# Performance work log

Hardware: AMD Instinct MI355X
Metric: run time of the kernel (lower is better)

Reference implementation:

```python
import jax, jax.numpy as jnp
import numpy as np

D, NH, NL, NP, NLAYERS, DFF = 256, 8, 4, 4, 6, 1024
DH = D // NH
SHAPES = [(96, 96), (48, 48), (24, 24), (12, 12)]
STARTS = np.concatenate([[0], np.cumsum([h * w for h, w in SHAPES])[:-1]]).tolist()
LQ = sum(h * w for h, w in SHAPES)
B = 2


def setup_inputs():
    ks = iter(jax.random.split(jax.random.key(0), 64))
    inp = {}
    for i, (h, w) in enumerate(SHAPES):
        inp[f"src{i}"] = jax.random.normal(next(ks), (B, D, h, w), jnp.float32)
        inp[f"pos{i}"] = jax.random.normal(next(ks), (B, D, h, w), jnp.float32) * 0.1
    inp["level_embed"] = jax.random.normal(next(ks), (NL, D), jnp.float32) * 0.02
    W = lambda s, sc: jax.random.normal(next(ks), s, jnp.float32) * sc
    inp["W_off"] = W((NLAYERS, D, NH * NL * NP * 2), 0.01)
    inp["b_off"] = W((NLAYERS, NH * NL * NP * 2), 0.5)
    inp["W_attn"] = W((NLAYERS, D, NH * NL * NP), 0.02)
    inp["b_attn"] = W((NLAYERS, NH * NL * NP), 0.02)
    inp["W_val"] = W((NLAYERS, D, D), 0.05)
    inp["b_val"] = jnp.zeros((NLAYERS, D), jnp.float32)
    inp["W_out"] = W((NLAYERS, D, D), 0.05)
    inp["b_out"] = jnp.zeros((NLAYERS, D), jnp.float32)
    inp["ln1_g"] = jnp.ones((NLAYERS, D), jnp.float32)
    inp["ln1_b"] = jnp.zeros((NLAYERS, D), jnp.float32)
    inp["W_ffn1"] = W((NLAYERS, D, DFF), 0.05)
    inp["b_ffn1"] = jnp.zeros((NLAYERS, DFF), jnp.float32)
    inp["W_ffn2"] = W((NLAYERS, DFF, D), 0.05)
    inp["b_ffn2"] = jnp.zeros((NLAYERS, D), jnp.float32)
    inp["ln2_g"] = jnp.ones((NLAYERS, D), jnp.float32)
    inp["ln2_b"] = jnp.zeros((NLAYERS, D), jnp.float32)
    return inp


def layer_norm(x, g, b):
    mu = x.mean(-1, keepdims=True)
    var = ((x - mu) ** 2).mean(-1, keepdims=True)
    return (x - mu) * jax.lax.rsqrt(var + 1e-5) * g + b


def reference_points():
    refs = []
    for h, w in SHAPES:
        ys = (jnp.arange(h, dtype=jnp.float32) + 0.5) / h
        xs = (jnp.arange(w, dtype=jnp.float32) + 0.5) / w
        gy, gx = jnp.meshgrid(ys, xs, indexing="ij")
        refs.append(jnp.stack([gx.reshape(-1), gy.reshape(-1)], -1))
    return jnp.concatenate(refs, 0)  # [LQ, 2] (x, y); valid_ratios==1 so level-independent


def bilinear(v, loc, H_, W_):
    # v: [B, H*W, NH, DH]; loc: [B, LQ, NH, NP, 2] normalized to [0,1]
    # matches F.grid_sample(mode='bilinear', padding_mode='zeros', align_corners=False)
    x = loc[..., 0] * W_ - 0.5
    y = loc[..., 1] * H_ - 0.5
    x0f, y0f = jnp.floor(x), jnp.floor(y)
    lx, ly = x - x0f, y - y0f
    x0, y0 = x0f.astype(jnp.int32), y0f.astype(jnp.int32)

    def g(xi, yi):
        valid = ((xi >= 0) & (xi < W_) & (yi >= 0) & (yi < H_)).astype(v.dtype)
        flat = jnp.clip(yi, 0, H_ - 1) * W_ + jnp.clip(xi, 0, W_ - 1)  # [B,LQ,NH,NP]
        idx = flat.transpose(0, 1, 3, 2).reshape(B, LQ * NP, NH)
        got = jnp.take_along_axis(v, jnp.broadcast_to(idx[..., None], (B, LQ * NP, NH, DH)), axis=1)
        got = got.reshape(B, LQ, NP, NH, DH).transpose(0, 1, 3, 2, 4)  # [B,LQ,NH,NP,DH]
        return got * valid[..., None]

    return (g(x0, y0) * ((1 - lx) * (1 - ly))[..., None]
            + g(x0 + 1, y0) * (lx * (1 - ly))[..., None]
            + g(x0, y0 + 1) * ((1 - lx) * ly)[..., None]
            + g(x0 + 1, y0 + 1) * (lx * ly)[..., None])


def reference(src0, src1, src2, src3, pos0, pos1, pos2, pos3, level_embed,
              W_off, b_off, W_attn, b_attn, W_val, b_val, W_out, b_out,
              ln1_g, ln1_b, W_ffn1, b_ffn1, W_ffn2, b_ffn2, ln2_g, ln2_b):
    srcs = [src0, src1, src2, src3]
    poss = [pos0, pos1, pos2, pos3]
    x = jnp.concatenate([s.reshape(B, D, -1).transpose(0, 2, 1) for s in srcs], 1)  # [B,LQ,D]
    pos = jnp.concatenate(
        [p.reshape(B, D, -1).transpose(0, 2, 1) + level_embed[i][None, None] for i, p in enumerate(poss)], 1)
    ref = reference_points()  # [LQ,2]
    norm = jnp.array([[w, h] for h, w in SHAPES], jnp.float32)  # [NL,2] = (W,H)

    for li in range(NLAYERS):
        q = x + pos
        off = (q @ W_off[li] + b_off[li]).reshape(B, LQ, NH, NL, NP, 2)
        attn = jax.nn.softmax((q @ W_attn[li] + b_attn[li]).reshape(B, LQ, NH, NL * NP), -1)
        attn = attn.reshape(B, LQ, NH, NL, NP)
        val = (x @ W_val[li] + b_val[li]).reshape(B, LQ, NH, DH)
        loc = ref[None, :, None, None, None, :] + off / norm[None, None, None, :, None, :]
        out = jnp.zeros((B, LQ, NH, DH), x.dtype)
        for l, (h, w) in enumerate(SHAPES):
            vl = val[:, STARTS[l]:STARTS[l] + h * w]
            sampled = bilinear(vl, loc[:, :, :, l], h, w)  # [B,LQ,NH,NP,DH]
            out = out + (sampled * attn[:, :, :, l, :, None]).sum(3)
        out = out.reshape(B, LQ, D) @ W_out[li] + b_out[li]
        x = layer_norm(x + out, ln1_g[li], ln1_b[li])
        ffn = jax.nn.relu(x @ W_ffn1[li] + b_ffn1[li]) @ W_ffn2[li] + b_ffn2[li]
        x = layer_norm(x + ffn, ln2_g[li], ln2_b[li])
    return x
```

## Files before the change

### kernel.cpp

```cpp
#include <hip/hip_runtime.h>
#include <stdint.h>

#define NHEAD  8
#define NLAYER 6
#define BATCH  2
#define LQ     12240
#define MTOK   (BATCH*LQ)
#define MPAD   24576

typedef __attribute__((ext_vector_type(8))) short bf16x8;
typedef __attribute__((ext_vector_type(4))) float f32x4;
typedef __attribute__((ext_vector_type(4))) short s16x4;

__device__ __forceinline__ unsigned short f2bf(float f) {
  union { float f; uint32_t u; } v; v.f = f;
  uint32_t u = v.u;
  uint32_t r = (u + 0x7fffu + ((u >> 16) & 1u)) >> 16;
  return (unsigned short)r;
}
__device__ __forceinline__ float bf2f(unsigned short s) {
  union { uint32_t u; float f; } v; v.u = ((uint32_t)s) << 16;
  return v.f;
}

template<int EPI, int BM>
__global__ __launch_bounds__(256)
void gemm_kernel(const unsigned short* __restrict__ A,
                 const unsigned short* __restrict__ BT,
                 const float* __restrict__ bias,
                 float* __restrict__ Cf,
                 unsigned short* __restrict__ Cb,
                 int K, int ldc)
{
  constexpr int MT = BM / 32;
  __shared__ unsigned short lA[BM*64];
  __shared__ unsigned short lB[128*64];
  const int tid  = threadIdx.x;
  const int lane = tid & 63;
  const int wm = ((tid >> 6) >> 1) * (BM/2);
  const int wn = ((tid >> 6) & 1) * 64;
  const size_t row0 = (size_t)blockIdx.x * BM;
  const size_t col0 = (size_t)blockIdx.y * 128;

  f32x4 acc[MT][4] = {};

  for (int kt = 0; kt < K; kt += 64) {
#pragma unroll
    for (int i = 0; i < MT; ++i) {
      const int slot = i*256 + tid;
      const int r  = slot >> 3;
      const int cs = (slot & 7) ^ (r & 7);
      const unsigned short* ga = A + (row0 + r) * (size_t)K + kt + cs*8;
      __builtin_amdgcn_global_load_lds(
          (const __attribute__((address_space(1))) uint32_t*)ga,
          (__attribute__((address_space(3))) uint32_t*)(&lA[slot*8]), 16, 0, 0);
    }
#pragma unroll
    for (int i = 0; i < 4; ++i) {
      const int slot = i*256 + tid;
      const int r  = slot >> 3;
      const int cs = (slot & 7) ^ (r & 7);
      const unsigned short* gb = BT + (col0 + r) * (size_t)K + kt + cs*8;
      __builtin_amdgcn_global_load_lds(
          (const __attribute__((address_space(1))) uint32_t*)gb,
          (__attribute__((address_space(3))) uint32_t*)(&lB[slot*8]), 16, 0, 0);
    }
    __syncthreads();
#pragma unroll
    for (int kk = 0; kk < 2; ++kk) {
      bf16x8 af[MT], bfv[4];
#pragma unroll
      for (int m = 0; m < MT; ++m) {
        const int r  = wm + m*16 + (lane & 15);
        const int ch = (kk*4 + (lane >> 4)) ^ (r & 7);
        af[m] = *(const bf16x8*)(&lA[r*64 + ch*8]);
      }
#pragma unroll
      for (int n = 0; n < 4; ++n) {
        const int r  = wn + n*16 + (lane & 15);
        const int ch = (kk*4 + (lane >> 4)) ^ (r & 7);
        bfv[n] = *(const bf16x8*)(&lB[r*64 + ch*8]);
      }
#pragma unroll
      for (int m = 0; m < MT; ++m)
#pragma unroll
        for (int n = 0; n < 4; ++n)
          acc[m][n] = __builtin_amdgcn_mfma_f32_16x16x32_bf16(af[m], bfv[n], acc[m][n], 0, 0, 0);
    }
    __syncthreads();
  }

  const int lq = lane >> 4;
  const int lr = lane & 15;
#pragma unroll
  for (int n = 0; n < 4; ++n) {
    const int col = (int)col0 + wn + n*16 + lr;
    const float bv = bias ? bias[col] : 0.f;
#pragma unroll
    for (int m = 0; m < MT; ++m) {
      const size_t rb = row0 + wm + m*16 + lq*4;
#pragma unroll
      for (int i = 0; i < 4; ++i) {
        float v = acc[m][n][i] + bv;
        if (EPI == 2) v = fmaxf(v, 0.f);
        if (EPI == 0) Cf[(rb + i) * (size_t)ldc + col] = v;
        else          Cb[(rb + i) * (size_t)ldc + col] = f2bf(v);
      }
    }
  }
}

template<int MODE>
__global__ __launch_bounds__(256)
void gemm_ln_kernel(const unsigned short* __restrict__ A,
                    const unsigned short* __restrict__ BT,
                    const float* __restrict__ bias,
                    const float* __restrict__ xres,
                    const float* __restrict__ g,
                    const float* __restrict__ bn,
                    const unsigned short* __restrict__ posbf,
                    float* __restrict__ xoutf,
                    unsigned short* __restrict__ xbf,
                    unsigned short* __restrict__ qbf,
                    float* __restrict__ dout,
                    int K)
{
  __shared__ unsigned short lA[32*64];
  __shared__ unsigned short lB[256*64];
  __shared__ float rs1[4][32];
  __shared__ float rs2[4][32];
  const int tid  = threadIdx.x;
  const int lane = tid & 63;
  const int w    = tid >> 6;
  const size_t row0 = (size_t)blockIdx.x * 32;

  f32x4 acc[2][4] = {};

  for (int kt = 0; kt < K; kt += 64) {
    {
      const int slot = tid;
      const int r  = slot >> 3;
      const int cs = (slot & 7) ^ (r & 7);
      const unsigned short* ga = A + (row0 + r) * (size_t)K + kt + cs*8;
      __builtin_amdgcn_global_load_lds(
          (const __attribute__((address_space(1))) uint32_t*)ga,
          (__attribute__((address_space(3))) uint32_t*)(&lA[slot*8]), 16, 0, 0);
    }
#pragma unroll
    for (int i = 0; i < 8; ++i) {
      const int slot = i*256 + tid;
      const int r  = slot >> 3;
      const int cs = (slot & 7) ^ (r & 7);
      const unsigned short* gb = BT + (size_t)r * K + kt + cs*8;
      __builtin_amdgcn_global_load_lds(
          (const __attribute__((address_space(1))) uint32_t*)gb,
          (__attribute__((address_space(3))) uint32_t*)(&lB[slot*8]), 16, 0, 0);
    }
    __syncthreads();
#pragma unroll
    for (int kk = 0; kk < 2; ++kk) {
      bf16x8 af[2], bfv[4];
#pragma unroll
      for (int m = 0; m < 2; ++m) {
        const int r  = m*16 + (lane & 15);
        const int ch = (kk*4 + (lane >> 4)) ^ (r & 7);
        af[m] = *(const bf16x8*)(&lA[r*64 + ch*8]);
      }
#pragma unroll
      for (int n = 0; n < 4; ++n) {
        const int r  = w*64 + n*16 + (lane & 15);
        const int ch = (kk*4 + (lane >> 4)) ^ (r & 7);
        bfv[n] = *(const bf16x8*)(&lB[r*64 + ch*8]);
      }
#pragma unroll
      for (int m = 0; m < 2; ++m)
#pragma unroll
        for (int n = 0; n < 4; ++n)
          acc[m][n] = __builtin_amdgcn_mfma_f32_16x16x32_bf16(af[m], bfv[n], acc[m][n], 0, 0, 0);
    }
    __syncthreads();
  }

  const int lq = lane >> 4;
  const int lr = lane & 15;
  float bcol[4], gcol[4], bncol[4];
#pragma unroll
  for (int n = 0; n < 4; ++n) {
    const int c = w*64 + n*16 + lr;
    bcol[n]  = bias[c];
    gcol[n]  = g[c];
    bncol[n] = bn[c];
  }
#pragma unroll
  for (int m = 0; m < 2; ++m)
#pragma unroll
    for (int i = 0; i < 4; ++i) {
      const size_t row = row0 + m*16 + lq*4 + i;
#pragma unroll
      for (int n = 0; n < 4; ++n)
        acc[m][n][i] += bcol[n] + xres[row*256 + w*64 + n*16 + lr];
    }
#pragma unroll
  for (int m = 0; m < 2; ++m)
#pragma unroll
    for (int i = 0; i < 4; ++i) {
      float t1 = acc[m][0][i] + acc[m][1][i] + acc[m][2][i] + acc[m][3][i];
      float t2 = acc[m][0][i]*acc[m][0][i] + acc[m][1][i]*acc[m][1][i]
               + acc[m][2][i]*acc[m][2][i] + acc[m][3][i]*acc[m][3][i];
#pragma unroll
      for (int o = 1; o < 16; o <<= 1) {
        t1 += __shfl_xor(t1, o, 64);
        t2 += __shfl_xor(t2, o, 64);
      }
      if (lr == 0) {
        rs1[w][m*16 + lq*4 + i] = t1;
        rs2[w][m*16 + lq*4 + i] = t2;
      }
    }
  __syncthreads();
#pragma unroll
  for (int m = 0; m < 2; ++m)
#pragma unroll
    for (int i = 0; i < 4; ++i) {
      const int r = m*16 + lq*4 + i;
      const float s1 = rs1[0][r] + rs1[1][r] + rs1[2][r] + rs1[3][r];
      const float s2 = rs2[0][r] + rs2[1][r] + rs2[2][r] + rs2[3][r];
      const float mu  = s1 * (1.f/256.f);
      const float var = s2 * (1.f/256.f) - mu*mu;
      const float rstd = rsqrtf(var + 1e-5f);
      const size_t row = row0 + r;
#pragma unroll
      for (int n = 0; n < 4; ++n) {
        const int c = w*64 + n*16 + lr;
        const float nv = (acc[m][n][i] - mu) * rstd * gcol[n] + bncol[n];
        const size_t idx = row*256 + c;
        if (MODE == 2) {
          if (row < MTOK) dout[idx] = nv;
        } else {
          xoutf[idx] = nv;
          xbf[idx]   = f2bf(nv);
          if (MODE == 1) qbf[idx] = f2bf(nv + bf2f(posbf[idx]));
        }
      }
    }
}

__global__ void pack_kernel(const float* __restrict__ s0, const float* __restrict__ s1,
                            const float* __restrict__ s2, const float* __restrict__ s3,
                            const float* __restrict__ p0, const float* __restrict__ p1,
                            const float* __restrict__ p2, const float* __restrict__ p3,
                            const float* __restrict__ lev,
                            float* __restrict__ xo, unsigned short* __restrict__ po)
{
  const int bt = blockIdx.x;
  int lvl, st;
  if      (bt < 288) { lvl = 0; st = bt; }
  else if (bt < 360) { lvl = 1; st = bt - 288; }
  else if (bt < 378) { lvl = 2; st = bt - 360; }
  else               { lvl = 3; st = bt - 378; }
  const int HWs[4] = {9216, 2304, 576, 144};
  const int LSs[4] = {0, 9216, 11520, 12096};
  const int hw = HWs[lvl], ls = LSs[lvl];
  const int b = blockIdx.z & 1, isp = blockIdx.z >> 1;
  const float* ins[8] = {s0, s1, s2, s3, p0, p1, p2, p3};
  const float* in = ins[isp*4 + lvl];
  const int sbase = st*32, d0 = blockIdx.y*32;
  __shared__ float tile[32][33];
  const int tx = threadIdx.x, ty = threadIdx.y;
#pragma unroll
  for (int j = 0; j < 4; ++j) {
    int ss = sbase + tx;
    int dd = d0 + ty + j*8;
    tile[ty + j*8][tx] = (ss < hw) ? in[((size_t)b*256 + dd)*hw + ss] : 0.f;
  }
  __syncthreads();
  const float addv = isp ? lev[lvl*256 + d0 + tx] : 0.f;
#pragma unroll
  for (int j = 0; j < 4; ++j) {
    int ss = sbase + ty + j*8;
    if (ss < hw) {
      const size_t idx = (size_t)(b*LQ + ls + ss)*256 + d0 + tx;
      const float v = tile[tx][ty + j*8] + addv;
      if (isp) po[idx] = f2bf(v);
      else     xo[idx] = v;
    }
  }
}

__global__ void wtrans_kernel(const float* __restrict__ Woff, const float* __restrict__ Watt,
                              const float* __restrict__ Wval, const float* __restrict__ Wout,
                              const float* __restrict__ Wf1,  const float* __restrict__ Wf2,
                              unsigned short* __restrict__ WoaT, unsigned short* __restrict__ WvalT,
                              unsigned short* __restrict__ WoutT, unsigned short* __restrict__ Wf1T,
                              unsigned short* __restrict__ Wf2T)
{
  const int li = blockIdx.z;
  const int bt = blockIdx.x;
  const float* in; unsigned short* out; int Kd, Nd, tn, tIdx;
  if      (bt < 64)  { in = Woff + (size_t)li*65536;  out = WoaT  + (size_t)li*98304;         Kd=256;  Nd=256;  tn=8;  tIdx=bt; }
  else if (bt < 96)  { in = Watt + (size_t)li*32768;  out = WoaT  + (size_t)li*98304 + 65536; Kd=256;  Nd=128;  tn=4;  tIdx=bt-64; }
  else if (bt < 160) { in = Wval + (size_t)li*65536;  out = WvalT + (size_t)li*65536;         Kd=256;  Nd=256;  tn=8;  tIdx=bt-96; }
  else if (bt < 224) { in = Wout + (size_t)li*65536;  out = WoutT + (size_t)li*65536;         Kd=256;  Nd=256;  tn=8;  tIdx=bt-160; }
  else if (bt < 480) { in = Wf1  + (size_t)li*262144; out = Wf1T  + (size_t)li*262144;        Kd=256;  Nd=1024; tn=32; tIdx=bt-224; }
  else               { in = Wf2  + (size_t)li*262144; out = Wf2T  + (size_t)li*262144;        Kd=1024; Nd=256;  tn=8;  tIdx=bt-480; }
  const int kt = tIdx / tn, nt = tIdx - kt*tn;
  const int k0 = kt*32, n0 = nt*32;
  __shared__ float tile[32][33];
  const int tx = threadIdx.x, ty = threadIdx.y;
#pragma unroll
  for (int j = 0; j < 4; ++j)
    tile[ty + j*8][tx] = in[(size_t)(k0 + ty + j*8) * Nd + n0 + tx];
  __syncthreads();
#pragma unroll
  for (int j = 0; j < 4; ++j)
    out[(size_t)(n0 + ty + j*8) * Kd + k0 + tx] = f2bf(tile[tx][ty + j*8]);
}

__global__ void bias_concat_kernel(const float* __restrict__ boff, const float* __restrict__ batt,
                                   float* __restrict__ boa)
{
  const int li = blockIdx.x, i = threadIdx.x;
  boa[li*384 + i] = (i < 256) ? boff[li*256 + i] : batt[li*128 + (i - 256)];
}

__global__ void prep_kernel(const float* __restrict__ x, const unsigned short* __restrict__ posbf,
                            unsigned short* __restrict__ xbf, unsigned short* __restrict__ qbf)
{
  const int idx = blockIdx.x * 256 + threadIdx.x;
  const int row = idx >> 6;
  s16x4 xb = {}, qb = {};
  if (row < MTOK) {
    const f32x4 xv = *(const f32x4*)(x + (size_t)idx*4);
    const s16x4 pv = *(const s16x4*)(posbf + (size_t)idx*4);
#pragma unroll
    for (int j = 0; j < 4; ++j) {
      xb[j] = (short)f2bf(xv[j]);
      qb[j] = (short)f2bf(xv[j] + bf2f((unsigned short)pv[j]));
    }
  }
  *(s16x4*)(xbf + (size_t)idx*4) = xb;
  *(s16x4*)(qbf + (size_t)idx*4) = qb;
}

__global__ __launch_bounds__(256)
void sample_kernel(const unsigned short* __restrict__ Coab, const float* __restrict__ valf,
                   unsigned short* __restrict__ outbf)
{
  __shared__ int4  pdo[32][17];
  __shared__ f32x4 pdw[32][17];
  const int tid = threadIdx.x;
  const int gi  = tid >> 3;
  const int g   = blockIdx.x * 32 + gi;
  const int t   = g >> 3, h = g & 7;
  const int b   = (t >= LQ) ? 1 : 0;

  {
    const int i0 = tid & 7;
    int4  ov0 = {0,0,0,0}, ov1 = {0,0,0,0};
    f32x4 wv0 = {0,0,0,0}, wv1 = {0,0,0,0};
    if (t < MTOK) {
      const int q = t - b * LQ;
      float refx, refy;
      if      (q < 9216)  { const int r = q;         const int rw = r/96; refx = (r - rw*96 + 0.5f)*(1.f/96.f); refy = (rw + 0.5f)*(1.f/96.f); }
      else if (q < 11520) { const int r = q - 9216;  const int rw = r/48; refx = (r - rw*48 + 0.5f)*(1.f/48.f); refy = (rw + 0.5f)*(1.f/48.f); }
      else if (q < 12096) { const int r = q - 11520; const int rw = r/24; refx = (r - rw*24 + 0.5f)*(1.f/24.f); refy = (rw + 0.5f)*(1.f/24.f); }
      else                { const int r = q - 12096; const int rw = r/12; refx = (r - rw*12 + 0.5f)*(1.f/12.f); refy = (rw + 0.5f)*(1.f/12.f); }
      const size_t crow = (size_t)t * 384;
      const float l0 = bf2f(Coab[crow + 256 + h*16 + i0]);
      const float l1 = bf2f(Coab[crow + 256 + h*16 + i0 + 8]);
      float mx = fmaxf(l0, l1);
#pragma unroll
      for (int m = 1; m < 8; m <<= 1) mx = fmaxf(mx, __shfl_xor(mx, m, 64));
      const float e0 = __expf(l0 - mx), e1 = __expf(l1 - mx);
      float sum = e0 + e1;
#pragma unroll
      for (int m = 1; m < 8; m <<= 1) sum += __shfl_xor(sum, m, 64);
      const float inv = 1.f / sum;

      auto mkpd = [&](int i, float aw, int4& ov, f32x4& wv) {
        const int l    = i >> 2;
        const int wl   = (l == 0) ? 96 : (l == 1) ? 48 : (l == 2) ? 24 : 12;
        const int base = (l == 0) ? 0  : (l == 1) ? 9216 : (l == 2) ? 11520 : 12096;
        const float ox = bf2f(Coab[crow + h*32 + 2*i]);
        const float oy = bf2f(Coab[crow + h*32 + 2*i + 1]);
        const float fw = (float)wl;
        const float xx = refx*fw + ox - 0.5f;
        const float yy = refy*fw + oy - 0.5f;
        const float xf = floorf(xx), yf = floorf(yy);
        const int x0 = (int)xf, y0 = (int)yf;
        const float lx = xx - xf, ly = yy - yf;
        const bool vx0 = (x0   >= 0) & (x0   < wl);
        const bool vx1 = (x0+1 >= 0) & (x0+1 < wl);
        const bool vy0 = (y0   >= 0) & (y0   < wl);
        const bool vy1 = (y0+1 >= 0) & (y0+1 < wl);
        const int cx0 = min(max(x0,   0), wl-1);
        const int cx1 = min(max(x0+1, 0), wl-1);
        const int cy0 = min(max(y0,   0), wl-1);
        const int cy1 = min(max(y0+1, 0), wl-1);
        ov.x = (base + cy0*wl + cx0) * 1024;
        ov.y = (base + cy0*wl + cx1) * 1024;
        ov.z = (base + cy1*wl + cx0) * 1024;
        ov.w = (base + cy1*wl + cx1) * 1024;
        wv[0] = (vx0 & vy0) ? (1.f-lx)*(1.f-ly)*aw : 0.f;
        wv[1] = (vx1 & vy0) ? lx*(1.f-ly)*aw       : 0.f;
        wv[2] = (vx0 & vy1) ? (1.f-lx)*ly*aw       : 0.f;
        wv[3] = (vx1 & vy1) ? lx*ly*aw             : 0.f;
      };
      mkpd(i0,     e0 * inv, ov0, wv0);
      mkpd(i0 + 8, e1 * inv, ov1, wv1);
    }
    pdo[gi][i0]     = ov0;  pdw[gi][i0]     = wv0;
    pdo[gi][i0 + 8] = ov1;  pdw[gi][i0 + 8] = wv1;
  }
  __syncthreads();

  const int lane8 = tid & 7;
  const char* vb = (const char*)(valf + (size_t)b*LQ*256 + h*32 + lane8*4);
  const int4*  po8 = pdo[gi];
  const f32x4* pw8 = pdw[gi];
  f32x4 a0 = {}, a1 = {}, a2 = {}, a3 = {};
#pragma unroll
  for (int p = 0; p < 16; ++p) {
    const int4  o = po8[p];
    const f32x4 w = pw8[p];
    const f32x4 c0 = *(const f32x4*)(vb + o.x);
    const f32x4 c1 = *(const f32x4*)(vb + o.y);
    const f32x4 c2 = *(const f32x4*)(vb + o.z);
    const f32x4 c3 = *(const f32x4*)(vb + o.w);
    a0 += c0 * w[0];
    a1 += c1 * w[1];
    a2 += c2 * w[2];
    a3 += c3 * w[3];
  }
  const f32x4 s = (a0 + a1) + (a2 + a3);
  s16x4 ob;
#pragma unroll
  for (int j = 0; j < 4; ++j) ob[j] = (short)f2bf(s[j]);
  *(s16x4*)(outbf + (size_t)t*256 + h*32 + lane8*4) = ob;
}

extern "C" void kernel_launch(void* const* d_in, const int* in_sizes, int n_in,
                              void* d_out, int out_size, void* d_ws, size_t ws_size,
                              hipStream_t stream)
{
  const float* src0 = (const float*)d_in[0];
  const float* pos0 = (const float*)d_in[1];
  const float* src1 = (const float*)d_in[2];
  const float* pos1 = (const float*)d_in[3];
  const float* src2 = (const float*)d_in[4];
  const float* pos2 = (const float*)d_in[5];
  const float* src3 = (const float*)d_in[6];
  const float* pos3 = (const float*)d_in[7];
  const float* lev  = (const float*)d_in[8];
  const float* W_off= (const float*)d_in[9];
  const float* b_off= (const float*)d_in[10];
  const float* W_att= (const float*)d_in[11];
  const float* b_att= (const float*)d_in[12];
  const float* W_val= (const float*)d_in[13];
  const float* b_val= (const float*)d_in[14];
  const float* W_out= (const float*)d_in[15];
  const float* b_out= (const float*)d_in[16];
  const float* ln1g = (const float*)d_in[17];
  const float* ln1b = (const float*)d_in[18];
  const float* W_f1 = (const float*)d_in[19];
  const float* b_f1 = (const float*)d_in[20];
  const float* W_f2 = (const float*)d_in[21];
  const float* b_f2 = (const float*)d_in[22];
  const float* ln2g = (const float*)d_in[23];
  const float* ln2b = (const float*)d_in[24];

  char* wp = (char*)d_ws;
  auto take = [&](size_t bytes) { char* p = wp; wp += (bytes + 255) & ~(size_t)255; return p; };
  float* x    = (float*)take((size_t)MPAD*256*4);
  float* valf = (float*)take((size_t)MPAD*256*4);
  unsigned short* posbf  = (unsigned short*)take((size_t)MPAD*256*2);
  unsigned short* Coab   = (unsigned short*)take((size_t)MPAD*384*2);
  unsigned short* xbf    = (unsigned short*)take((size_t)MPAD*256*2);
  unsigned short* qbf    = (unsigned short*)take((size_t)MPAD*256*2);
  unsigned short* sampbf = (unsigned short*)take((size_t)MPAD*256*2);
  unsigned short* h1bf   = (unsigned short*)take((size_t)MPAD*1024*2);
  unsigned short* WoaT   = (unsigned short*)take((size_t)NLAYER*384*256*2);
  unsigned short* WvalT  = (unsigned short*)take((size_t)NLAYER*256*256*2);
  unsigned short* WoutT  = (unsigned short*)take((size_t)NLAYER*256*256*2);
  unsigned short* Wf1T   = (unsigned short*)take((size_t)NLAYER*1024*256*2);
  unsigned short* Wf2T   = (unsigned short*)take((size_t)NLAYER*256*1024*2);
  float* boa  = (float*)take((size_t)NLAYER*384*4);

  dim3 tb(32, 8);
  pack_kernel<<<dim3(383, 8, 4), tb, 0, stream>>>(src0, src1, src2, src3,
                                                  pos0, pos1, pos2, pos3, lev, x, posbf);
  wtrans_kernel<<<dim3(736, 1, 6), tb, 0, stream>>>(W_off, W_att, W_val, W_out, W_f1, W_f2,
                                                    WoaT, WvalT, WoutT, Wf1T, Wf2T);
  bias_concat_kernel<<<NLAYER, 384, 0, stream>>>(b_off, b_att, boa);
  prep_kernel<<<MPAD/4, 256, 0, stream>>>(x, posbf, xbf, qbf);

  for (int li = 0; li < NLAYER; ++li) {
    gemm_kernel<1,64><<<dim3(MPAD/64, 3), 256, 0, stream>>>(qbf, WoaT + (size_t)li*98304,
        boa + li*384, nullptr, Coab, 256, 384);
    gemm_kernel<0,64><<<dim3(MPAD/64, 2), 256, 0, stream>>>(xbf, WvalT + (size_t)li*65536,
        b_val + li*256, valf, nullptr, 256, 256);
    sample_kernel<<<MPAD/4, 256, 0, stream>>>(Coab, valf, sampbf);
    gemm_ln_kernel<0><<<MPAD/32, 256, 0, stream>>>(sampbf, WoutT + (size_t)li*65536,
        b_out + li*256, x, ln1g + li*256, ln1b + li*256, nullptr,
        x, xbf, nullptr, nullptr, 256);
    gemm_kernel<2,128><<<dim3(MPAD/128, 8), 256, 0, stream>>>(xbf, Wf1T + (size_t)li*262144,
        b_f1 + li*1024, nullptr, h1bf, 256, 1024);
    if (li < NLAYER-1)
      gemm_ln_kernel<1><<<MPAD/32, 256, 0, stream>>>(h1bf, Wf2T + (size_t)li*262144,
          b_f2 + li*256, x, ln2g + li*256, ln2b + li*256, posbf,
          x, xbf, qbf, nullptr, 1024);
    else
      gemm_ln_kernel<2><<<MPAD/32, 256, 0, stream>>>(h1bf, Wf2T + (size_t)li*262144,
          b_f2 + li*256, x, ln2g + li*256, ln2b + li*256, nullptr,
          nullptr, nullptr, nullptr, (float*)d_out, 1024);
  }
}
```

Before: 974.2 us.

## Fuse FFN up-projection, ReLU, down-projection and LayerNorm into one kernel

Adds an ffn_ln_kernel in which each 32-row block computes the 1024-wide hidden activation in 256-column chunks. Each chunk goes through ReLU into shared memory and is immediately multiplied by W2, before the residual and LayerNorm epilogue. This removes the separate FFN1 GEMM launch and the write and read of the bf16 hidden buffer in global memory. In exchange, every block re-streams the full W1 and W2 for the layer through L2, and about 64 KB of LDS per block is used with no double buffering, which may lower occupancy. The old templated gemm_ln is simplified to handle only the attention output path.

```diff
diff --git a/kernel.cpp b/kernel.cpp
--- a/kernel.cpp
+++ b/kernel.cpp
@@ -21,6 +21,11 @@
 __device__ __forceinline__ float bf2f(unsigned short s) {
   union { uint32_t u; float f; } v; v.u = ((uint32_t)s) << 16;
   return v.f;
+}
+__device__ __forceinline__ void gll16(const unsigned short* g, unsigned short* l) {
+  __builtin_amdgcn_global_load_lds(
+      (const __attribute__((address_space(1))) uint32_t*)g,
+      (__attribute__((address_space(3))) uint32_t*)l, 16, 0, 0);
 }
 
 template<int EPI, int BM>
@@ -50,20 +55,14 @@
       const int slot = i*256 + tid;
       const int r  = slot >> 3;
       const int cs = (slot & 7) ^ (r & 7);
-      const unsigned short* ga = A + (row0 + r) * (size_t)K + kt + cs*8;
-      __builtin_amdgcn_global_load_lds(
-          (const __attribute__((address_space(1))) uint32_t*)ga,
-          (__attribute__((address_space(3))) uint32_t*)(&lA[slot*8]), 16, 0, 0);
+      gll16(A + (row0 + r) * (size_t)K + kt + cs*8, &lA[slot*8]);
     }
 #pragma unroll
     for (int i = 0; i < 4; ++i) {
       const int slot = i*256 + tid;
       const int r  = slot >> 3;
       const int cs = (slot & 7) ^ (r & 7);
-      const unsigned short* gb = BT + (col0 + r) * (size_t)K + kt + cs*8;
-      __builtin_amdgcn_global_load_lds(
-          (const __attribute__((address_space(1))) uint32_t*)gb,
-          (__attribute__((address_space(3))) uint32_t*)(&lB[slot*8]), 16, 0, 0);
+      gll16(BT + (col0 + r) * (size_t)K + kt + cs*8, &lB[slot*8]);
     }
     __syncthreads();
 #pragma unroll
@@ -110,7 +109,6 @@
   }
 }
 
-template<int MODE>
 __global__ __launch_bounds__(256)
 void gemm_ln_kernel(const unsigned short* __restrict__ A,
                     const unsigned short* __restrict__ BT,
@@ -118,11 +116,8 @@
                     const float* __restrict__ xres,
                     const float* __restrict__ g,
                     const float* __restrict__ bn,
-                    const unsigned short* __restrict__ posbf,
                     float* __restrict__ xoutf,
                     unsigned short* __restrict__ xbf,
-                    unsigned short* __restrict__ qbf,
-                    float* __restrict__ dout,
                     int K)
 {
   __shared__ unsigned short lA[32*64];
@@ -141,20 +136,14 @@
       const int slot = tid;
       const int r  = slot >> 3;
       const int cs = (slot & 7) ^ (r & 7);
-      const unsigned short* ga = A + (row0 + r) * (size_t)K + kt + cs*8;
-      __builtin_amdgcn_global_load_lds(
-          (const __attribute__((address_space(1))) uint32_t*)ga,
-          (__attribute__((address_space(3))) uint32_t*)(&lA[slot*8]), 16, 0, 0);
+      gll16(A + (row0 + r) * (size_t)K + kt + cs*8, &lA[slot*8]);
     }
 #pragma unroll
     for (int i = 0; i < 8; ++i) {
       const int slot = i*256 + tid;
       const int r  = slot >> 3;
       const int cs = (slot & 7) ^ (r & 7);
-      const unsigned short* gb = BT + (size_t)r * K + kt + cs*8;
-      __builtin_amdgcn_global_load_lds(
-          (const __attribute__((address_space(1))) uint32_t*)gb,
-          (__attribute__((address_space(3))) uint32_t*)(&lB[slot*8]), 16, 0, 0);
+      gll16(BT + (size_t)r * K + kt + cs*8, &lB[slot*8]);
     }
     __syncthreads();
 #pragma unroll
@@ -234,12 +223,191 @@
         const int c = w*64 + n*16 + lr;
         const float nv = (acc[m][n][i] - mu) * rstd * gcol[n] + bncol[n];
         const size_t idx = row*256 + c;
+        xoutf[idx] = nv;
+        xbf[idx]   = f2bf(nv);
+      }
+    }
+}
+
+template<int MODE>
+__global__ __launch_bounds__(256)
+void ffn_ln_kernel(const unsigned short* __restrict__ xbfin,
+                   const unsigned short* __restrict__ W1T,
+                   const unsigned short* __restrict__ W2T,
+                   const float* __restrict__ b1,
+                   const float* __restrict__ bias,
+                   const float* __restrict__ xres,
+                   const float* __restrict__ g,
+                   const float* __restrict__ bn,
+                   const unsigned short* __restrict__ posbf,
+                   float* __restrict__ xoutf,
+                   unsigned short* __restrict__ xbf,
+                   unsigned short* __restrict__ qbf,
+                   float* __restrict__ dout)
+{
+  __shared__ unsigned short lX[32*256];
+  __shared__ unsigned short lH[32*256];
+  __shared__ unsigned short lB[256*64];
+  __shared__ float rs1[4][32];
+  __shared__ float rs2[4][32];
+  const int tid  = threadIdx.x;
+  const int lane = tid & 63;
+  const int w    = tid >> 6;
+  const int lq   = lane >> 4;
+  const int lr   = lane & 15;
+  const size_t row0 = (size_t)blockIdx.x * 32;
+
+#pragma unroll
+  for (int i = 0; i < 4; ++i) {
+    const int slot = i*256 + tid;
+    const int r  = slot >> 5;
+    const int cl = slot & 31;
+    const int cs = cl ^ (r & 7);
+    gll16(xbfin + (row0 + r) * 256 + cs*8, &lX[slot*8]);
+  }
+
+  f32x4 acc2[2][4] = {};
+
+  for (int nc = 0; nc < 4; ++nc) {
+    f32x4 acc1[2][4] = {};
+#pragma unroll
+    for (int kt = 0; kt < 4; ++kt) {
+#pragma unroll
+      for (int i = 0; i < 8; ++i) {
+        const int slot = i*256 + tid;
+        const int r  = slot >> 3;
+        const int cs = (slot & 7) ^ (r & 7);
+        gll16(W1T + (size_t)(nc*256 + r) * 256 + kt*64 + cs*8, &lB[slot*8]);
+      }
+      __syncthreads();
+#pragma unroll
+      for (int kk = 0; kk < 2; ++kk) {
+        bf16x8 af[2], bfv[4];
+#pragma unroll
+        for (int m = 0; m < 2; ++m) {
+          const int r = m*16 + (lane & 15);
+          const int c = (kt*8 + kk*4 + (lane >> 4)) ^ (r & 7);
+          af[m] = *(const bf16x8*)(&lX[r*256 + c*8]);
+        }
+#pragma unroll
+        for (int n = 0; n < 4; ++n) {
+          const int r  = w*64 + n*16 + (lane & 15);
+          const int ch = (kk*4 + (lane >> 4)) ^ (r & 7);
+          bfv[n] = *(const bf16x8*)(&lB[r*64 + ch*8]);
+        }
+#pragma unroll
+        for (int m = 0; m < 2; ++m)
+#pragma unroll
+          for (int n = 0; n < 4; ++n)
+            acc1[m][n] = __builtin_amdgcn_mfma_f32_16x16x32_bf16(af[m], bfv[n], acc1[m][n], 0, 0, 0);
+      }
+      __syncthreads();
+    }
+#pragma unroll
+    for (int n = 0; n < 4; ++n) {
+      const int kcol = w*64 + n*16 + lr;
+      const float bv = b1[nc*256 + kcol];
+      const int c = kcol >> 3, e = kcol & 7;
+#pragma unroll
+      for (int m = 0; m < 2; ++m)
+#pragma unroll
+        for (int i = 0; i < 4; ++i) {
+          const int r = m*16 + lq*4 + i;
+          lH[r*256 + (c ^ (r & 7))*8 + e] = f2bf(fmaxf(acc1[m][n][i] + bv, 0.f));
+        }
+    }
+#pragma unroll
+    for (int kt = 0; kt < 4; ++kt) {
+#pragma unroll
+      for (int i = 0; i < 8; ++i) {
+        const int slot = i*256 + tid;
+        const int r  = slot >> 3;
+        const int cs = (slot & 7) ^ (r & 7);
+        gll16(W2T + (size_t)r * 1024 + nc*256 + kt*64 + cs*8, &lB[slot*8]);
+      }
+      __syncthreads();
+#pragma unroll
+      for (int kk = 0; kk < 2; ++kk) {
+        bf16x8 af[2], bfv[4];
+#pragma unroll
+        for (int m = 0; m < 2; ++m) {
+          const int r = m*16 + (lane & 15);
+          const int c = (kt*8 + kk*4 + (lane >> 4)) ^ (r & 7);
+          af[m] = *(const bf16x8*)(&lH[r*256 + c*8]);
+        }
+#pragma unroll
+        for (int n = 0; n < 4; ++n) {
+          const int r  = w*64 + n*16 + (lane & 15);
+          const int ch = (kk*4 + (lane >> 4)) ^ (r & 7);
+          bfv[n] = *(const bf16x8*)(&lB[r*64 + ch*8]);
+        }
+#pragma unroll
+        for (int m = 0; m < 2; ++m)
+#pragma unroll
+          for (int n = 0; n < 4; ++n)
+            acc2[m][n] = __builtin_amdgcn_mfma_f32_16x16x32_bf16(af[m], bfv[n], acc2[m][n], 0, 0, 0);
+      }
+      __syncthreads();
+    }
+  }
+
+  float bcol[4], gcol[4], bncol[4];
+#pragma unroll
+  for (int n = 0; n < 4; ++n) {
+    const int c = w*64 + n*16 + lr;
+    bcol[n]  = bias[c];
+    gcol[n]  = g[c];
+    bncol[n] = bn[c];
+  }
+#pragma unroll
+  for (int m = 0; m < 2; ++m)
+#pragma unroll
+    for (int i = 0; i < 4; ++i) {
+      const size_t row = row0 + m*16 + lq*4 + i;
+#pragma unroll
+      for (int n = 0; n < 4; ++n)
+        acc2[m][n][i] += bcol[n] + xres[row*256 + w*64 + n*16 + lr];
+    }
+#pragma unroll
+  for (int m = 0; m < 2; ++m)
+#pragma unroll
+    for (int i = 0; i < 4; ++i) {
+      float t1 = acc2[m][0][i] + acc2[m][1][i] + acc2[m][2][i] + acc2[m][3][i];
+      float t2 = acc2[m][0][i]*acc2[m][0][i] + acc2[m][1][i]*acc2[m][1][i]
+               + acc2[m][2][i]*acc2[m][2][i] + acc2[m][3][i]*acc2[m][3][i];
+#pragma unroll
+      for (int o = 1; o < 16; o <<= 1) {
+        t1 += __shfl_xor(t1, o, 64);
+        t2 += __shfl_xor(t2, o, 64);
+      }
+      if (lr == 0) {
+        rs1[w][m*16 + lq*4 + i] = t1;
+        rs2[w][m*16 + lq*4 + i] = t2;
+      }
+    }
+  __syncthreads();
+#pragma unroll
+  for (int m = 0; m < 2; ++m)
+#pragma unroll
+    for (int i = 0; i < 4; ++i) {
+      const int r = m*16 + lq*4 + i;
+      const float s1 = rs1[0][r] + rs1[1][r] + rs1[2][r] + rs1[3][r];
+      const float s2 = rs2[0][r] + rs2[1][r] + rs2[2][r] + rs2[3][r];
+      const float mu  = s1 * (1.f/256.f);
+      const float var = s2 * (1.f/256.f) - mu*mu;
+      const float rstd = rsqrtf(var + 1e-5f);
+      const size_t row = row0 + r;
+#pragma unroll
+      for (int n = 0; n < 4; ++n) {
+        const int c = w*64 + n*16 + lr;
+        const float nv = (acc2[m][n][i] - mu) * rstd * gcol[n] + bncol[n];
+        const size_t idx = row*256 + c;
         if (MODE == 2) {
           if (row < MTOK) dout[idx] = nv;
         } else {
           xoutf[idx] = nv;
           xbf[idx]   = f2bf(nv);
-          if (MODE == 1) qbf[idx] = f2bf(nv + bf2f(posbf[idx]));
+          qbf[idx]   = f2bf(nv + bf2f(posbf[idx]));
         }
       }
     }
@@ -478,7 +646,6 @@
   unsigned short* xbf    = (unsigned short*)take((size_t)MPAD*256*2);
   unsigned short* qbf    = (unsigned short*)take((size_t)MPAD*256*2);
   unsigned short* sampbf = (unsigned short*)take((size_t)MPAD*256*2);
-  unsigned short* h1bf   = (unsigned short*)take((size_t)MPAD*1024*2);
   unsigned short* WoaT   = (unsigned short*)take((size_t)NLAYER*384*256*2);
   unsigned short* WvalT  = (unsigned short*)take((size_t)NLAYER*256*256*2);
   unsigned short* WoutT  = (unsigned short*)take((size_t)NLAYER*256*256*2);
@@ -500,18 +667,17 @@
     gemm_kernel<0,64><<<dim3(MPAD/64, 2), 256, 0, stream>>>(xbf, WvalT + (size_t)li*65536,
         b_val + li*256, valf, nullptr, 256, 256);
     sample_kernel<<<MPAD/4, 256, 0, stream>>>(Coab, valf, sampbf);
-    gemm_ln_kernel<0><<<MPAD/32, 256, 0, stream>>>(sampbf, WoutT + (size_t)li*65536,
-        b_out + li*256, x, ln1g + li*256, ln1b + li*256, nullptr,
-        x, xbf, nullptr, nullptr, 256);
-    gemm_kernel<2,128><<<dim3(MPAD/128, 8), 256, 0, stream>>>(xbf, Wf1T + (size_t)li*262144,
-        b_f1 + li*1024, nullptr, h1bf, 256, 1024);
+    gemm_ln_kernel<<<MPAD/32, 256, 0, stream>>>(sampbf, WoutT + (size_t)li*65536,
+        b_out + li*256, x, ln1g + li*256, ln1b + li*256, x, xbf, 256);
     if (li < NLAYER-1)
-      gemm_ln_kernel<1><<<MPAD/32, 256, 0, stream>>>(h1bf, Wf2T + (size_t)li*262144,
-          b_f2 + li*256, x, ln2g + li*256, ln2b + li*256, posbf,
-          x, xbf, qbf, nullptr, 1024);
+      ffn_ln_kernel<1><<<MPAD/32, 256, 0, stream>>>(xbf,
+          Wf1T + (size_t)li*262144, Wf2T + (size_t)li*262144,
+          b_f1 + li*1024, b_f2 + li*256, x, ln2g + li*256, ln2b + li*256,
+          posbf, x, xbf, qbf, nullptr);
     else
-      gemm_ln_kernel<2><<<MPAD/32, 256, 0, stream>>>(h1bf, Wf2T + (size_t)li*262144,
-          b_f2 + li*256, x, ln2g + li*256, ln2b + li*256, nullptr,
-          nullptr, nullptr, nullptr, (float*)d_out, 1024);
-  }
-}
+      ffn_ln_kernel<2><<<MPAD/32, 256, 0, stream>>>(xbf,
+          Wf1T + (size_t)li*262144, Wf2T + (size_t)li*262144,
+          b_f1 + li*1024, b_f2 + li*256, x, ln2g + li*256, ln2b + li*256,
+          nullptr, nullptr, nullptr, nullptr, (float*)d_out);
+  }
+}
```

Result: slower. 1.031 ms (+5.9%).
